# Optimization experiments

Hardware: AMD Instinct MI355X
Metric: run time of the kernel (lower is better)

## Reference

```python
import jax, jax.numpy as jnp
import numpy as np

EPS = 1e-5


def _lstm(x, W_ih, W_hh, b_ih, b_hh):
    # x: [B, T, in]; torch LSTM gate order i, f, g, o. Returns (last h, last c).
    def step(carry, xt):
        h, c = carry
        z = xt @ W_ih.T + h @ W_hh.T + (b_ih + b_hh)  # [B, 4H]
        i, f, g, o = jnp.split(z, 4, axis=-1)
        c = jax.nn.sigmoid(f) * c + jax.nn.sigmoid(i) * jnp.tanh(g)
        h = jax.nn.sigmoid(o) * jnp.tanh(c)
        return (h, c), None
    h0 = jnp.zeros((x.shape[0], W_hh.shape[1]), x.dtype)
    (h, c), _ = jax.lax.scan(step, (h0, h0), jnp.swapaxes(x, 0, 1))
    return h, c


def _bn_train(x, g, b):
    # BatchNorm1d in training mode: batch stats, biased variance.
    m = x.mean(axis=0)
    v = x.var(axis=0)
    return g * (x - m) * jax.lax.rsqrt(v + EPS) + b


def _forward(agent_traj, neighbours, aW_ih, aW_hh, ab_ih, ab_hh,
             nW_ih, nW_hh, nb_ih, nb_hh, dW_ih, dW_hh, db_ih, db_hh,
             pW, pb, rW, rb, m1W, m1b, g1, be1, m2W, m2b, g2, be2,
             i1W, i1b, ig1, ib1, i2W, i2b, ig2, ib2, segment_ids):
    B = agent_traj.shape[0]
    # relative distance: neighbour last position - owning agent's last position
    rel = neighbours[:, -1, :] - agent_traj[segment_ids, -1, :]          # [N, 2]
    agent_h, agent_c = _lstm(agent_traj, aW_ih, aW_hh, ab_ih, ab_hh)     # [B, 64]
    neigh_h, _ = _lstm(neighbours, nW_ih, nW_hh, nb_ih, nb_hh)           # [N, 64]
    rel_emb = rel @ rW.T + rb                                            # [N, 64]
    x = jnp.concatenate([neigh_h, rel_emb], axis=1)                      # [N, 128]
    x = _bn_train(jax.nn.relu(x @ m1W.T + m1b), g1, be1)                 # [N, 512]
    x = _bn_train(jax.nn.relu(x @ m2W.T + m2b), g2, be2)                 # [N, 1024]
    # per-sample max pooling over each sample's neighbours (zeros if none)
    pooled = jax.ops.segment_max(x, segment_ids, num_segments=B)         # [B, 1024]
    counts = jax.ops.segment_sum(jnp.ones((x.shape[0],), x.dtype), segment_ids, num_segments=B)
    pooled = jnp.where(counts[:, None] > 0, pooled, jnp.zeros((), x.dtype))
    d = jnp.concatenate([pooled, agent_h], axis=1)                       # [B, 1088]
    d = _bn_train(jax.nn.relu(d @ i1W.T + i1b), ig1, ib1)                # [B, 1024]
    d = _bn_train(jax.nn.relu(d @ i2W.T + i2b), ig2, ib2)                # [B, 64]

    def dec_step(carry, _):
        h, c = carry
        z = h @ dW_ih.T + h @ dW_hh.T + (db_ih + db_hh)
        i, f, g, o = jnp.split(z, 4, axis=-1)
        c = jax.nn.sigmoid(f) * c + jax.nn.sigmoid(i) * jnp.tanh(g)
        h = jax.nn.sigmoid(o) * jnp.tanh(c)
        return (h, c), h
    _, hs = jax.lax.scan(dec_step, (d, agent_c), None, length=30)        # [30, B, 64]
    pred = jnp.einsum('tbh,oh->bto', hs, pW) + pb                        # [B, 30, 2]
    return pred


def setup_inputs() -> dict:
    B, T, N, Tn, H = 2048, 20, 32768, 20, 64
    key = jax.random.key(0)
    ki = iter(jax.random.split(key, 40))
    def rn(shape, s=0.1):
        return jax.random.normal(next(ki), shape, dtype=jnp.float32) * s
    inp = dict(
        agent_traj=rn((B, T, 2), 1.0),
        neighbours=rn((N, Tn, 2), 1.0),
        aW_ih=rn((4 * H, 2)), aW_hh=rn((4 * H, H)), ab_ih=rn((4 * H,)), ab_hh=rn((4 * H,)),
        nW_ih=rn((4 * H, 2)), nW_hh=rn((4 * H, H)), nb_ih=rn((4 * H,)), nb_hh=rn((4 * H,)),
        dW_ih=rn((4 * H, H)), dW_hh=rn((4 * H, H)), db_ih=rn((4 * H,)), db_hh=rn((4 * H,)),
        pW=rn((2, H)), pb=rn((2,)),
        rW=rn((H, 2)), rb=rn((H,)),
        m1W=rn((512, 128)), m1b=rn((512,)),
        g1=jnp.ones((512,), jnp.float32), be1=jnp.zeros((512,), jnp.float32),
        m2W=rn((1024, 512)), m2b=rn((1024,)),
        g2=jnp.ones((1024,), jnp.float32), be2=jnp.zeros((1024,), jnp.float32),
        i1W=rn((1024, 1088)), i1b=rn((1024,)),
        ig1=jnp.ones((1024,), jnp.float32), ib1=jnp.zeros((1024,), jnp.float32),
        i2W=rn((H, 1024)), i2b=rn((H,)),
        ig2=jnp.ones((H,), jnp.float32), ib2=jnp.zeros((H,), jnp.float32),
        segment_ids=jnp.sort(jax.random.randint(next(ki), (N,), 0, B)).astype(jnp.int32),
    )
    return inp


def reference(agent_traj, neighbours, aW_ih, aW_hh, ab_ih, ab_hh,
              nW_ih, nW_hh, nb_ih, nb_hh, dW_ih, dW_hh, db_ih, db_hh,
              pW, pb, rW, rb, m1W, m1b, g1, be1, m2W, m2b, g2, be2,
              i1W, i1b, ig1, ib1, i2W, i2b, ig2, ib2, segment_ids):
    return _forward(agent_traj, neighbours, aW_ih, aW_hh, ab_ih, ab_hh,
                    nW_ih, nW_hh, nb_ih, nb_hh, dW_ih, dW_hh, db_ih, db_hh,
                    pW, pb, rW, rb, m1W, m1b, g1, be1, m2W, m2b, g2, be2,
                    i1W, i1b, ig1, ib1, i2W, i2b, ig2, ib2, segment_ids)
```

## Files before the change

kernel.cpp:

```cpp
#include <hip/hip_runtime.h>

#define EPS_BN 1e-5f

typedef __attribute__((ext_vector_type(8))) short short8;
typedef __attribute__((ext_vector_type(4))) float f32x4;

__device__ __forceinline__ float fast_rcp(float x) { return __builtin_amdgcn_rcpf(x); }
__device__ __forceinline__ float sigmoid_f(float x) { return fast_rcp(1.0f + __expf(-x)); }
__device__ __forceinline__ float tanh_f(float x) { return 1.0f - 2.0f * fast_rcp(__expf(2.0f * x) + 1.0f); }

__device__ __forceinline__ unsigned short f2bf(float f) {
    unsigned u = __float_as_uint(f);
    u += 0x7FFFu + ((u >> 16) & 1u);
    return (unsigned short)(u >> 16);
}
__device__ __forceinline__ unsigned pk_bf(float a, float b) {
    return (unsigned)f2bf(a) | ((unsigned)f2bf(b) << 16);
}
__device__ __forceinline__ float bf_hi(float f) {
    return __uint_as_float((unsigned)f2bf(f) << 16);
}
__device__ __forceinline__ float bf2f(unsigned short u) {
    return __uint_as_float((unsigned)u << 16);
}

__device__ __forceinline__ void gload16(const unsigned short* g, unsigned short* l) {
    __builtin_amdgcn_global_load_lds(
        (const __attribute__((address_space(1))) unsigned int*)g,
        (__attribute__((address_space(3))) unsigned int*)l,
        16, 0, 0);
}

union AFrag { short e[8]; short8 v; };
union BFrag { uint4 u; short8 v; };

__global__ __launch_bounds__(256, 2) void lstm_mfma(
    const float* __restrict__ xA,
    const float* __restrict__ aW_ih, const float* __restrict__ aW_hh,
    const float* __restrict__ ab_ih, const float* __restrict__ ab_hh,
    float* __restrict__ agent_h, float* __restrict__ agent_c,
    const float* __restrict__ xN,
    const float* __restrict__ nW_ih, const float* __restrict__ nW_hh,
    const float* __restrict__ nb_ih, const float* __restrict__ nb_hh,
    float* __restrict__ neigh_h,
    int nAgentBlk, int T)
{
    __shared__ unsigned h_ex[2][2][32 * 52];

    const bool isA = (blockIdx.x < (unsigned)nAgentBlk);
    const long blk = isA ? blockIdx.x : blockIdx.x - nAgentBlk;
    const float* __restrict__ x     = isA ? xA   : xN;
    const float* __restrict__ W_ih  = isA ? aW_ih : nW_ih;
    const float* __restrict__ W_hh  = isA ? aW_hh : nW_hh;
    const float* __restrict__ b_ih  = isA ? ab_ih : nb_ih;
    const float* __restrict__ b_hh  = isA ? ab_hh : nb_hh;
    float* __restrict__ h_out = isA ? agent_h : neigh_h;
    float* __restrict__ c_out = isA ? agent_c : nullptr;

    const int tid  = threadIdx.x;
    const int w    = tid >> 6;
    const int lane = tid & 63;
    const int s    = lane & 15;
    const int q    = lane >> 4;

    short8 ahi[4][3], alo[4][3];
#pragma unroll
    for (int gt = 0; gt < 4; ++gt) {
        const int n = gt * 64 + w * 16 + s;
#pragma unroll
        for (int kc = 0; kc < 2; ++kc) {
            const float* src = &W_hh[n * 64 + kc * 32 + q * 8];
            float4 v0 = *(const float4*)src;
            float4 v1 = *(const float4*)(src + 4);
            float v[8] = {v0.x, v0.y, v0.z, v0.w, v1.x, v1.y, v1.z, v1.w};
            AFrag a, b;
#pragma unroll
            for (int j = 0; j < 8; ++j) {
                a.e[j] = (short)f2bf(v[j]);
                b.e[j] = (short)f2bf(v[j] - bf_hi(v[j]));
            }
            ahi[gt][kc] = a.v;
            alo[gt][kc] = b.v;
        }
        AFrag a2, b2;
#pragma unroll
        for (int j = 0; j < 8; ++j) { a2.e[j] = 0; b2.e[j] = 0; }
        if (q == 0) {
            const float wi0 = W_ih[n * 2 + 0];
            const float wi1 = W_ih[n * 2 + 1];
            const float bs  = b_ih[n] + b_hh[n];
            a2.e[0] = (short)f2bf(wi0); b2.e[0] = (short)f2bf(wi0 - bf_hi(wi0));
            a2.e[1] = (short)f2bf(wi1); b2.e[1] = (short)f2bf(wi1 - bf_hi(wi1));
            a2.e[2] = (short)f2bf(bs);  b2.e[2] = (short)f2bf(bs  - bf_hi(bs));
        }
        ahi[gt][2] = a2.v;
        alo[gt][2] = b2.v;
    }

    for (int i = tid; i < 2 * 2 * 32 * 52; i += 256) (&h_ex[0][0][0])[i] = 0u;
    __syncthreads();
    if (tid < 32) {
        h_ex[0][0][tid * 52 + 33] = pk_bf(1.0f, 0.0f);
        h_ex[1][0][tid * 52 + 33] = pk_bf(1.0f, 0.0f);
        float2 xv = *(const float2*)&x[(blk * 32 + tid) * (long)(T * 2)];
        h_ex[0][0][tid * 52 + 32] = pk_bf(xv.x, xv.y);
        h_ex[0][1][tid * 52 + 32] = pk_bf(xv.x - bf_hi(xv.x), xv.y - bf_hi(xv.y));
    }
    __syncthreads();

    float creg[2][4] = {{0.f, 0.f, 0.f, 0.f}, {0.f, 0.f, 0.f, 0.f}};

    for (int t = 0; t < T; ++t) {
        const int rb = t & 1, wb = rb ^ 1;
        BFrag bhi[2][3], blo[2][3];
#pragma unroll
        for (int g = 0; g < 2; ++g)
#pragma unroll
        for (int kc = 0; kc < 3; ++kc) {
            const int off = (g * 16 + s) * 52 + kc * 16 + (q >> 1) * 8 + (q & 1) * 4;
            bhi[g][kc].u = *(const uint4*)&h_ex[rb][0][off];
            blo[g][kc].u = *(const uint4*)&h_ex[rb][1][off];
        }

        f32x4 acc[4][2];
#pragma unroll
        for (int gt = 0; gt < 4; ++gt) { acc[gt][0] = (f32x4)0.f; acc[gt][1] = (f32x4)0.f; }

#pragma unroll
        for (int kc = 0; kc < 3; ++kc) {
#pragma unroll
            for (int g = 0; g < 2; ++g) {
                const short8 bh = bhi[g][kc].v;
                const short8 bl = blo[g][kc].v;
#pragma unroll
                for (int gt = 0; gt < 4; ++gt) {
                    f32x4 a = acc[gt][g];
                    a = __builtin_amdgcn_mfma_f32_16x16x32_bf16(ahi[gt][kc], bh, a, 0, 0, 0);
                    a = __builtin_amdgcn_mfma_f32_16x16x32_bf16(ahi[gt][kc], bl, a, 0, 0, 0);
                    a = __builtin_amdgcn_mfma_f32_16x16x32_bf16(alo[gt][kc], bh, a, 0, 0, 0);
                    acc[gt][g] = a;
                }
            }
        }

#pragma unroll
        for (int g = 0; g < 2; ++g) {
            float hval[4];
#pragma unroll
            for (int r = 0; r < 4; ++r) {
                const float ei = __expf(-acc[0][g][r]);
                const float eg = __expf(2.0f * acc[2][g][r]);
                const float it = (eg - 1.0f) * fast_rcp((1.0f + ei) * (eg + 1.0f));
                const float sf = fast_rcp(1.0f + __expf(-acc[1][g][r]));
                const float c  = fmaf(sf, creg[g][r], it);
                creg[g][r] = c;
                const float eo = __expf(-acc[3][g][r]);
                const float ec = __expf(2.0f * c);
                hval[r] = (ec - 1.0f) * fast_rcp((1.0f + eo) * (ec + 1.0f));
            }
            {
                const int w0 = (g * 16 + s) * 52 + w * 8 + q * 2;
                h_ex[wb][0][w0]     = pk_bf(hval[0], hval[1]);
                h_ex[wb][0][w0 + 1] = pk_bf(hval[2], hval[3]);
                h_ex[wb][1][w0]     = pk_bf(hval[0] - bf_hi(hval[0]), hval[1] - bf_hi(hval[1]));
                h_ex[wb][1][w0 + 1] = pk_bf(hval[2] - bf_hi(hval[2]), hval[3] - bf_hi(hval[3]));
            }
            if (t == T - 1) {
                const long seq = blk * 32 + g * 16 + s;
                const int j0 = w * 16 + q * 4;
                *(float4*)&h_out[seq * 64 + j0] = make_float4(hval[0], hval[1], hval[2], hval[3]);
                if (c_out)
                    *(float4*)&c_out[seq * 64 + j0] =
                        make_float4(creg[g][0], creg[g][1], creg[g][2], creg[g][3]);
            }
        }
        if (tid < 32 && t + 1 < T) {
            float2 xv = *(const float2*)&x[(blk * 32 + tid) * (long)(T * 2) + (t + 1) * 2];
            h_ex[wb][0][tid * 52 + 32] = pk_bf(xv.x, xv.y);
            h_ex[wb][1][tid * 52 + 32] = pk_bf(xv.x - bf_hi(xv.x), xv.y - bf_hi(xv.y));
        }
        __syncthreads();
    }
}

__global__ __launch_bounds__(256) void build_x0(
    const float* __restrict__ neigh_h, const float* __restrict__ neighbours,
    const float* __restrict__ agent_traj, const int* __restrict__ seg,
    const float* __restrict__ rW, const float* __restrict__ rb,
    unsigned short* __restrict__ x0hi, unsigned short* __restrict__ x0lo, int T)
{
    const long n = (long)blockIdx.x * 2 + (threadIdx.x >> 7);
    const int j = threadIdx.x & 127;
    float v;
    if (j < 64) {
        v = neigh_h[n*64 + j];
    } else {
        const int o = j - 64;
        const int sid = seg[n];
        const float ra = neighbours[n*(long)(T*2) + (T-1)*2 + 0] - agent_traj[(long)sid*(T*2) + (T-1)*2 + 0];
        const float rbv= neighbours[n*(long)(T*2) + (T-1)*2 + 1] - agent_traj[(long)sid*(T*2) + (T-1)*2 + 1];
        v = fmaf(rW[o*2+0], ra, fmaf(rW[o*2+1], rbv, rb[o]));
    }
    x0hi[n*128 + j] = f2bf(v);
    x0lo[n*128 + j] = f2bf(v - bf_hi(v));
}

__global__ __launch_bounds__(64) void prep_wfrag(
    const float* __restrict__ W, const float* __restrict__ sc, int K,
    unsigned short* __restrict__ Whi, unsigned short* __restrict__ Wlo)
{
    const int nKc = K >> 5;
    const int blk = blockIdx.x;
    const int ti = blk / nKc, kc = blk - ti * nKc;
    const int l = threadIdx.x;
    const int n = ti * 16 + (l & 15);
    const int k0 = kc * 32 + (l >> 4) * 8;
    const long ob = ((long)blk * 64 + l) * 8;
#pragma unroll
    for (int j = 0; j < 8; ++j) {
        float v = W[(long)n * K + k0 + j];
        if (sc) v *= sc[k0 + j];
        Whi[ob + j] = f2bf(v);
        Wlo[ob + j] = f2bf(v - bf_hi(v));
    }
}

__global__ __launch_bounds__(64) void prep_bias(
    const float* __restrict__ W, const float* __restrict__ sh,
    const float* __restrict__ b, int K, float* __restrict__ bout)
{
    const int n = blockIdx.x;
    const int l = threadIdx.x;
    float s = 0.f;
    if (sh)
        for (int k = l; k < K; k += 64) s += sh[k] * W[(long)n * K + k];
#pragma unroll
    for (int m = 32; m >= 1; m >>= 1) s += __shfl_xor(s, m, 64);
    if (l == 0) bout[n] = b[n] + s;
}

__global__ __launch_bounds__(256, 2) void gemm_split(
    const unsigned short* __restrict__ Ahi,
    const unsigned short* __restrict__ Alo,
    const unsigned short* __restrict__ Whi,
    const unsigned short* __restrict__ Wlo,
    const float* __restrict__ bias,
    float* __restrict__ Yf,
    unsigned short* __restrict__ Yhi,
    unsigned short* __restrict__ Ylo,
    float* __restrict__ accum,
    const int* __restrict__ segp,
    float* __restrict__ poolmax,
    int M, int K, int O)
{
    __shared__ unsigned short As[2][2][128 * 32];
    __shared__ int segl[128];
    const int t = threadIdx.x;
    const int lane = t & 63;
    const int w = t >> 6;
    const int wm = w & 1, wn = w >> 1;

    const int nx = gridDim.x;
    const int flat = blockIdx.y * nx + blockIdx.x;
    const int grp = flat / (8 * nx);
    const int loc = flat - grp * (8 * nx);
    const int m0 = (grp * 8 + (loc & 7)) * 128;
    const int n0 = (loc >> 3) * 128;
    const int nKc = K >> 5;

    f32x4 acc[4][4];
#pragma unroll
    for (int mt = 0; mt < 4; ++mt)
#pragma unroll
    for (int nt = 0; nt < 4; ++nt) acc[mt][nt] = (f32x4)0.f;

    const int rloc0 = w * 32 + (lane >> 2);
    const int rloc1 = rloc0 + 16;
    const int sd = lane & 3;
    const unsigned short* gsrc[2][2];
    gsrc[0][0] = Ahi + (long)(m0 + rloc0) * K + (sd ^ ((rloc0 >> 1) & 3)) * 8;
    gsrc[0][1] = Ahi + (long)(m0 + rloc1) * K + (sd ^ ((rloc1 >> 1) & 3)) * 8;
    gsrc[1][0] = Alo + (long)(m0 + rloc0) * K + (sd ^ ((rloc0 >> 1) & 3)) * 8;
    gsrc[1][1] = Alo + (long)(m0 + rloc1) * K + (sd ^ ((rloc1 >> 1) & 3)) * 8;

    auto stageA = [&](int buf, int kc) {
#pragma unroll
        for (int pp = 0; pp < 2; ++pp)
#pragma unroll
        for (int cc = 0; cc < 2; ++cc)
            gload16(gsrc[pp][cc] + kc * 32,
                    &As[buf][pp][(w * 32 + cc * 16) * 32]);
    };

    const int s2 = ((lane >> 4) ^ ((lane >> 1) & 3)) * 8;
    const int arow = wm * 64 + (lane & 15);
    const long bt0 = (long)((n0 >> 4) + wn * 4);

    auto loadB = [&](BFrag* bh, BFrag* bl, int kc) {
#pragma unroll
        for (int nt = 0; nt < 4; ++nt) {
            const long fb = ((bt0 + nt) * nKc + kc) * 512 + lane * 8;
            bh[nt].u = *(const uint4*)(Whi + fb);
            bl[nt].u = *(const uint4*)(Wlo + fb);
        }
    };
    auto compute = [&](int buf, BFrag* bh, BFrag* bl) {
        BFrag afh[4], afl[4];
#pragma unroll
        for (int mt = 0; mt < 4; ++mt) {
            afh[mt].u = *(const uint4*)&As[buf][0][(arow + mt * 16) * 32 + s2];
            afl[mt].u = *(const uint4*)&As[buf][1][(arow + mt * 16) * 32 + s2];
        }
#pragma unroll
        for (int nt = 0; nt < 4; ++nt)
#pragma unroll
        for (int mt = 0; mt < 4; ++mt) {
            f32x4 a = acc[mt][nt];
            a = __builtin_amdgcn_mfma_f32_16x16x32_bf16(afh[mt].v, bh[nt].v, a, 0, 0, 0);
            a = __builtin_amdgcn_mfma_f32_16x16x32_bf16(afh[mt].v, bl[nt].v, a, 0, 0, 0);
            a = __builtin_amdgcn_mfma_f32_16x16x32_bf16(afl[mt].v, bh[nt].v, a, 0, 0, 0);
            acc[mt][nt] = a;
        }
    };

    BFrag bh0[4], bl0[4], bh1[4], bl1[4];
    stageA(0, 0);
    loadB(bh0, bl0, 0);
    __syncthreads();
    for (int kc = 0; kc < nKc; kc += 2) {
        stageA(1, kc + 1);
        loadB(bh1, bl1, kc + 1);
        compute(0, bh0, bl0);
        __syncthreads();
        if (kc + 2 < nKc) {
            stageA(0, kc + 2);
            loadB(bh0, bl0, kc + 2);
        }
        compute(1, bh1, bl1);
        if (kc + 2 < nKc) __syncthreads();
    }

    int sid0 = 0, span = 0;
    bool useLds = false;
    float* pool = nullptr;
    if (segp) {
        __syncthreads();
        if (t < 128) segl[t] = segp[m0 + t];
        __syncthreads();
        sid0 = segl[0];
        span = segl[127] - sid0 + 1;
        pool = (float*)&As[0][0][0];
        useLds = (span <= 60);
        if (useLds) {
            for (int i = t; i < span * 132; i += 256) pool[i] = 0.f;
            __syncthreads();
        }
    }

    const int cn = lane & 15, cq = lane >> 4;
#pragma unroll
    for (int nt = 0; nt < 4; ++nt) {
        const int cl = wn * 64 + nt * 16 + cn;
        const int n = n0 + cl;
        const float bs = bias[n];
        float s = 0.f, ssq = 0.f;
#pragma unroll
        for (int mt = 0; mt < 4; ++mt) {
            const int mb = wm * 64 + mt * 16 + cq * 4;
            float vmax = 0.f; int sid = -1;
#pragma unroll
            for (int r = 0; r < 4; ++r) {
                const float v = fmaxf(acc[mt][nt][r] + bs, 0.f);
                s += v; ssq += v * v;
                if (segp) {
                    const int sr = segl[mb + r];
                    if (r == 0) { vmax = v; sid = sr; }
                    else if (sr == sid) { vmax = fmaxf(vmax, v); }
                    else {
                        if (vmax > 0.f) {
                            if (useLds)
                                atomicMax((int*)&pool[(sid - sid0) * 132 + cl], __float_as_int(vmax));
                            else
                                atomicMax((int*)&poolmax[(long)sid * O + n], __float_as_int(vmax));
                        }
                        sid = sr; vmax = v;
                    }
                } else if (Yf) {
                    Yf[(long)(m0 + mb + r) * O + n] = v;
                } else {
                    const long idx = (long)(m0 + mb + r) * O + n;
                    Yhi[idx] = f2bf(v);
                    Ylo[idx] = f2bf(v - bf_hi(v));
                }
            }
            if (segp && vmax > 0.f) {
                if (useLds)
                    atomicMax((int*)&pool[(sid - sid0) * 132 + cl], __float_as_int(vmax));
                else
                    atomicMax((int*)&poolmax[(long)sid * O + n], __float_as_int(vmax));
            }
        }
        if (accum) {
            s   += __shfl_xor(s, 16, 64);   ssq += __shfl_xor(ssq, 16, 64);
            s   += __shfl_xor(s, 32, 64);   ssq += __shfl_xor(ssq, 32, 64);
            if (cq == 0) {
                atomicAdd(&accum[n], s);
                atomicAdd(&accum[O + n], ssq);
            }
        }
    }

    if (segp && useLds) {
        __syncthreads();
        for (int e = t; e < span * 128; e += 256) {
            const int sl = e >> 7, c = e & 127;
            const float v = pool[sl * 132 + c];
            const long gi = (long)(sid0 + sl) * O + (n0 + c);
            if (sl == 0 || sl == span - 1) {
                if (v > 0.f) atomicMax((int*)&poolmax[gi], __float_as_int(v));
            } else {
                poolmax[gi] = v;
            }
        }
    }
}

__global__ __launch_bounds__(256) void colstats(
    const float* __restrict__ Y, int M, int O, int chunkRows,
    float* __restrict__ accum)
{
    const int c = blockIdx.x * 64 + (threadIdx.x & 63);
    const int rgrp = threadIdx.x >> 6;
    const int r0 = blockIdx.y * chunkRows;
    int rend = r0 + chunkRows; if (rend > M) rend = M;
    float s = 0.f, ss = 0.f;
    for (int r = r0 + rgrp; r < rend; r += 4) {
        const float v = Y[(long)r*O + c];
        s += v; ss += v*v;
    }
    __shared__ float l1[256], l2[256];
    l1[threadIdx.x] = s; l2[threadIdx.x] = ss;
    __syncthreads();
    if (threadIdx.x < 64) {
        const int c2 = blockIdx.x * 64 + threadIdx.x;
        s  = l1[threadIdx.x] + l1[threadIdx.x+64] + l1[threadIdx.x+128] + l1[threadIdx.x+192];
        ss = l2[threadIdx.x] + l2[threadIdx.x+64] + l2[threadIdx.x+128] + l2[threadIdx.x+192];
        atomicAdd(&accum[c2], s);
        atomicAdd(&accum[O + c2], ss);
    }
}

__global__ __launch_bounds__(256) void bn_finalize(
    const float* __restrict__ accum, const float* __restrict__ g,
    const float* __restrict__ be, int O, float invM,
    float* __restrict__ scale, float* __restrict__ shift)
{
    const int o = blockIdx.x * 256 + threadIdx.x;
    if (o < O) {
        const float mean = accum[o] * invM;
        const float var  = accum[O + o] * invM - mean * mean;
        const float sc   = g[o] * rsqrtf(var + EPS_BN);
        scale[o] = sc;
        shift[o] = be[o] - mean * sc;
    }
}

__global__ __launch_bounds__(256) void build_d0(
    const float* __restrict__ poolraw, const float* __restrict__ agent_h,
    const int* __restrict__ seg, int N,
    const float* __restrict__ sc2, const float* __restrict__ sh2,
    unsigned short* __restrict__ d0hi, unsigned short* __restrict__ d0lo)
{
    const int b = blockIdx.x;
    int l = 0, h = N;
    while (l < h) { const int mid = (l + h) >> 1; if (seg[mid] < b) l = mid + 1; else h = mid; }
    const bool nonempty = (l < N) && (seg[l] == b);
    for (int c = threadIdx.x; c < 1088; c += 256) {
        float v;
        if (c < 1024) {
            v = nonempty ? fmaf(sc2[c], poolraw[(long)b*1024 + c], sh2[c]) : 0.f;
        } else {
            v = agent_h[(long)b*64 + (c - 1024)];
        }
        d0hi[(long)b*1088 + c] = f2bf(v);
        d0lo[(long)b*1088 + c] = f2bf(v - bf_hi(v));
    }
}

__global__ __launch_bounds__(256) void gemm_i2_part(
    const float* __restrict__ A,
    const float* __restrict__ W,
    const float* __restrict__ ascale, const float* __restrict__ ashift,
    float* __restrict__ part, int M, int K, int kchunk)
{
    __shared__ float As[16][132];
    __shared__ float Bs[16][68];
    const int t = threadIdx.x;
    const int m0 = blockIdx.x * 128;
    const int ks = blockIdx.y;
    const int kbeg = ks * kchunk;
    const int kend = kbeg + kchunk;
    const int tm = (t & 15) * 8;
    const int tn = (t >> 4) * 4;
    const int ar = t >> 1;
    const int ac = (t & 1) * 8;
    const int br = t >> 2;
    const int bc = (t & 3) * 4;

    float acc[8][4];
#pragma unroll
    for (int i = 0; i < 8; ++i)
#pragma unroll
    for (int j = 0; j < 4; ++j) acc[i][j] = 0.f;

    for (int k0 = kbeg; k0 < kend; k0 += 16) {
        float4 a0 = *(const float4*)&A[(long)(m0+ar)*K + k0 + ac];
        float4 a1 = *(const float4*)&A[(long)(m0+ar)*K + k0 + ac + 4];
        float4 s0 = *(const float4*)&ascale[k0 + ac];
        float4 s1 = *(const float4*)&ascale[k0 + ac + 4];
        float4 h0 = *(const float4*)&ashift[k0 + ac];
        float4 h1 = *(const float4*)&ashift[k0 + ac + 4];
        a0.x = fmaf(a0.x, s0.x, h0.x); a0.y = fmaf(a0.y, s0.y, h0.y);
        a0.z = fmaf(a0.z, s0.z, h0.z); a0.w = fmaf(a0.w, s0.w, h0.w);
        a1.x = fmaf(a1.x, s1.x, h1.x); a1.y = fmaf(a1.y, s1.y, h1.y);
        a1.z = fmaf(a1.z, s1.z, h1.z); a1.w = fmaf(a1.w, s1.w, h1.w);
        float4 b0 = *(const float4*)&W[(long)br*K + k0 + bc];
        __syncthreads();
        As[ac+0][ar] = a0.x; As[ac+1][ar] = a0.y; As[ac+2][ar] = a0.z; As[ac+3][ar] = a0.w;
        As[ac+4][ar] = a1.x; As[ac+5][ar] = a1.y; As[ac+6][ar] = a1.z; As[ac+7][ar] = a1.w;
        Bs[bc+0][br] = b0.x; Bs[bc+1][br] = b0.y; Bs[bc+2][br] = b0.z; Bs[bc+3][br] = b0.w;
        __syncthreads();
#pragma unroll
        for (int kk = 0; kk < 16; ++kk) {
            float av[8], bv[4];
            *(float4*)&av[0] = *(const float4*)&As[kk][tm];
            *(float4*)&av[4] = *(const float4*)&As[kk][tm + 4];
            *(float4*)&bv[0] = *(const float4*)&Bs[kk][tn];
#pragma unroll
            for (int i = 0; i < 8; ++i)
#pragma unroll
            for (int j = 0; j < 4; ++j)
                acc[i][j] = fmaf(av[i], bv[j], acc[i][j]);
        }
    }

    float* po = part + (long)ks * M * 64;
#pragma unroll
    for (int i = 0; i < 8; ++i)
        *(float4*)&po[(long)(m0 + tm + i) * 64 + tn] = *(float4*)&acc[i][0];
}

__global__ __launch_bounds__(256) void i2_finish(
    const float* __restrict__ part, const float* __restrict__ bias,
    int M, int KS, float* __restrict__ t2)
{
    const long idx = (long)blockIdx.x * 256 + threadIdx.x;
    if (idx < (long)M * 64) {
        float s = 0.f;
        for (int ks = 0; ks < KS; ++ks) s += part[(long)ks * M * 64 + idx];
        t2[idx] = fmaxf(s + bias[idx & 63], 0.f);
    }
}

__global__ __launch_bounds__(256) void prep_dec(
    const float* __restrict__ dW_ih, const float* __restrict__ dW_hh,
    const float* __restrict__ db_ih, const float* __restrict__ db_hh,
    float* __restrict__ Wc, float* __restrict__ bc)
{
    const int idx = blockIdx.x * 256 + threadIdx.x;
    if (idx < 256*64) Wc[idx] = dW_ih[idx] + dW_hh[idx];
    else if (idx < 256*64 + 256) bc[idx - 256*64] = db_ih[idx - 256*64] + db_hh[idx - 256*64];
}

__global__ __launch_bounds__(256) void decoder_kernel(
    const float* __restrict__ t2, const float* __restrict__ sc4,
    const float* __restrict__ sh4, const float* __restrict__ agent_c,
    const float* __restrict__ Wc, const float* __restrict__ bc,
    const float* __restrict__ pW, const float* __restrict__ pb,
    float* __restrict__ pred )
{
    __shared__ float h_lds[2][64];
    __shared__ float zg_lds[2][64];
    __shared__ float zo_lds[2][64];
    const int t = threadIdx.x;
    const int lane = t & 63;
    const int wave = t >> 6;
    const int s = wave >> 1;
    const int role = wave & 1;
    const long seq = (long)blockIdx.x * 2 + s;

    const int r0 = role * 128 + lane;
    const int r1 = r0 + 64;
    float w0[64], w1[64];
#pragma unroll
    for (int k = 0; k < 64; k += 4) {
        float4 va = *(const float4*)&Wc[r0 * 64 + k];
        w0[k] = va.x; w0[k+1] = va.y; w0[k+2] = va.z; w0[k+3] = va.w;
        float4 vb = *(const float4*)&Wc[r1 * 64 + k];
        w1[k] = vb.x; w1[k+1] = vb.y; w1[k+2] = vb.z; w1[k+3] = vb.w;
    }
    const float bias0 = bc[r0];
    const float bias1 = bc[r1];
    const float pw0 = pW[lane], pw1 = pW[64 + lane];
    const float pb0 = pb[0], pb1 = pb[1];

    float c = agent_c[seq*64 + lane];
    if (role == 0)
        h_lds[s][lane] = fmaf(sc4[lane], t2[seq*64 + lane], sh4[lane]);
    __syncthreads();
    float hv = h_lds[s][lane];

    for (int step = 0; step < 30; ++step) {
        float z0 = bias0, z1 = bias1;
#pragma unroll
        for (int k = 0; k < 64; ++k) {
            float hk = __int_as_float(__builtin_amdgcn_readlane(__float_as_int(hv), k));
            z0 = fmaf(hk, w0[k], z0);
            z1 = fmaf(hk, w1[k], z1);
        }
        if (role == 1) { zg_lds[s][lane] = z0; zo_lds[s][lane] = z1; }
        __syncthreads();
        if (role == 0) {
            const float ig = sigmoid_f(z0);
            const float fg = sigmoid_f(z1);
            const float gg = tanh_f(zg_lds[s][lane]);
            const float og = sigmoid_f(zo_lds[s][lane]);
            c = fmaf(fg, c, ig * gg);
            h_lds[s][lane] = og * tanh_f(c);
        }
        __syncthreads();
        hv = h_lds[s][lane];
        if (role == 0) {
            float p0 = hv * pw0;
            float p1 = hv * pw1;
#pragma unroll
            for (int m = 32; m >= 1; m >>= 1) {
                p0 += __shfl_xor(p0, m, 64);
                p1 += __shfl_xor(p1, m, 64);
            }
            if (lane == 0) {
                pred[seq*60 + step*2 + 0] = p0 + pb0;
                pred[seq*60 + step*2 + 1] = p1 + pb1;
            }
        }
    }
}

extern "C" void kernel_launch(void* const* d_in, const int* in_sizes, int n_in,
                              void* d_out, int out_size, void* d_ws, size_t ws_size,
                              hipStream_t stream)
{
    const float* agent_traj = (const float*)d_in[0];
    const float* neighbours = (const float*)d_in[1];
    const float* aW_ih = (const float*)d_in[2];
    const float* aW_hh = (const float*)d_in[3];
    const float* ab_ih = (const float*)d_in[4];
    const float* ab_hh = (const float*)d_in[5];
    const float* nW_ih = (const float*)d_in[6];
    const float* nW_hh = (const float*)d_in[7];
    const float* nb_ih = (const float*)d_in[8];
    const float* nb_hh = (const float*)d_in[9];
    const float* dW_ih = (const float*)d_in[10];
    const float* dW_hh = (const float*)d_in[11];
    const float* db_ih = (const float*)d_in[12];
    const float* db_hh = (const float*)d_in[13];
    const float* pW = (const float*)d_in[14];
    const float* pb = (const float*)d_in[15];
    const float* rW = (const float*)d_in[16];
    const float* rb = (const float*)d_in[17];
    const float* m1W = (const float*)d_in[18];
    const float* m1b = (const float*)d_in[19];
    const float* g1  = (const float*)d_in[20];
    const float* be1 = (const float*)d_in[21];
    const float* m2W = (const float*)d_in[22];
    const float* m2b = (const float*)d_in[23];
    const float* g2  = (const float*)d_in[24];
    const float* be2 = (const float*)d_in[25];
    const float* i1W = (const float*)d_in[26];
    const float* i1b = (const float*)d_in[27];
    const float* ig1 = (const float*)d_in[28];
    const float* ib1 = (const float*)d_in[29];
    const float* i2W = (const float*)d_in[30];
    const float* i2b = (const float*)d_in[31];
    const float* ig2 = (const float*)d_in[32];
    const float* ib2 = (const float*)d_in[33];
    const int*   seg = (const int*)d_in[34];
    float* pred = (float*)d_out;

    const int B = 2048, T = 20, N = 32768;

    char* p = (char*)d_ws;
    auto alloc = [&](size_t bytes) -> char* {
        char* r = p; p += (bytes + 255) & ~(size_t)255; return r;
    };
    float* agent_h = (float*)alloc((size_t)B*64*4);
    float* agent_c = (float*)alloc((size_t)B*64*4);
    char* neigh_region = alloc((size_t)N*64*4);
    unsigned short* x0hi = (unsigned short*)alloc((size_t)N*128*2);
    unsigned short* x0lo = (unsigned short*)alloc((size_t)N*128*2);
    char* y1hi_region  = alloc((size_t)N*512*2);
    unsigned short* y1lo = (unsigned short*)alloc((size_t)N*512*2);
    float* poolraw = (float*)alloc((size_t)B*1024*4);
    float* accAll = (float*)alloc((size_t)(1024+2048+2048+128)*4);
    float* acc1 = accAll;
    float* acc2 = accAll + 1024;
    float* acc3 = accAll + 3072;
    float* acc4 = accAll + 5120;
    float* sc1 = (float*)alloc(512*4);  float* sh1 = (float*)alloc(512*4);
    float* sc2 = (float*)alloc(1024*4); float* sh2 = (float*)alloc(1024*4);
    float* sc3 = (float*)alloc(1024*4); float* sh3 = (float*)alloc(1024*4);
    float* sc4 = (float*)alloc(64*4);   float* sh4 = (float*)alloc(64*4);
    float* Wc = (float*)alloc(256*64*4);
    float* bc = (float*)alloc(256*4);
    unsigned short* W1hi = (unsigned short*)alloc((size_t)512*128*2);
    unsigned short* W1lo = (unsigned short*)alloc((size_t)512*128*2);
    unsigned short* W2hi = (unsigned short*)alloc((size_t)1024*512*2);
    unsigned short* W2lo = (unsigned short*)alloc((size_t)1024*512*2);
    unsigned short* Wi1hi = (unsigned short*)alloc((size_t)1024*1088*2);
    unsigned short* Wi1lo = (unsigned short*)alloc((size_t)1024*1088*2);
    float* b1f = (float*)alloc(512*4);
    float* b2f = (float*)alloc(1024*4);
    float* bi1f = (float*)alloc(1024*4);
    float* i2part = (float*)alloc((size_t)8*B*64*4);

    float* neigh_h = (float*)neigh_region;
    float* t1      = (float*)neigh_region;
    unsigned short* y1hi = (unsigned short*)y1hi_region;
    unsigned short* d0hi = (unsigned short*)y1hi_region;
    unsigned short* d0lo = d0hi + (size_t)B*1088;
    float* t2 = (float*)(y1hi_region + (size_t)2*B*1088*2);

    hipMemsetAsync(accAll, 0, (1024+2048+2048+128)*sizeof(float), stream);
    hipMemsetAsync(poolraw, 0, (size_t)B*1024*4, stream);

    prep_wfrag<<<(512/16)*(128/32), 64, 0, stream>>>(m1W, nullptr, 128, W1hi, W1lo);
    prep_bias<<<512, 64, 0, stream>>>(m1W, nullptr, m1b, 128, b1f);
    prep_wfrag<<<(1024/16)*(1088/32), 64, 0, stream>>>(i1W, nullptr, 1088, Wi1hi, Wi1lo);
    prep_bias<<<1024, 64, 0, stream>>>(i1W, nullptr, i1b, 1088, bi1f);
    prep_dec<<<65, 256, 0, stream>>>(dW_ih, dW_hh, db_ih, db_hh, Wc, bc);

    lstm_mfma<<<B/32 + N/32, 256, 0, stream>>>(
        agent_traj, aW_ih, aW_hh, ab_ih, ab_hh, agent_h, agent_c,
        neighbours, nW_ih, nW_hh, nb_ih, nb_hh, neigh_h,
        B/32, T);
    build_x0<<<N/2, 256, 0, stream>>>(neigh_h, neighbours, agent_traj, seg, rW, rb,
                                      x0hi, x0lo, T);

    gemm_split<<<dim3(512/128, N/128), 256, 0, stream>>>(
        x0hi, x0lo, W1hi, W1lo, b1f, nullptr, y1hi, y1lo, acc1,
        nullptr, nullptr, N, 128, 512);
    bn_finalize<<<2, 256, 0, stream>>>(acc1, g1, be1, 512, 1.0f/N, sc1, sh1);

    prep_wfrag<<<(1024/16)*(512/32), 64, 0, stream>>>(m2W, sc1, 512, W2hi, W2lo);
    prep_bias<<<1024, 64, 0, stream>>>(m2W, sh1, m2b, 512, b2f);

    gemm_split<<<dim3(1024/128, N/128), 256, 0, stream>>>(
        y1hi, y1lo, W2hi, W2lo, b2f, nullptr, nullptr, nullptr, acc2,
        seg, poolraw, N, 512, 1024);
    bn_finalize<<<4, 256, 0, stream>>>(acc2, g2, be2, 1024, 1.0f/N, sc2, sh2);

    build_d0<<<B, 256, 0, stream>>>(poolraw, agent_h, seg, N, sc2, sh2, d0hi, d0lo);

    gemm_split<<<dim3(1024/128, B/128), 256, 0, stream>>>(
        d0hi, d0lo, Wi1hi, Wi1lo, bi1f, t1, nullptr, nullptr, acc3,
        nullptr, nullptr, B, 1088, 1024);
    bn_finalize<<<4, 256, 0, stream>>>(acc3, ig1, ib1, 1024, 1.0f/B, sc3, sh3);

    gemm_i2_part<<<dim3(B/128, 8), 256, 0, stream>>>(t1, i2W, sc3, sh3, i2part,
                                                     B, 1024, 128);
    i2_finish<<<(B*64)/256, 256, 0, stream>>>(i2part, i2b, B, 8, t2);
    colstats<<<dim3(1, 8), 256, 0, stream>>>(t2, B, 64, 256, acc4);
    bn_finalize<<<1, 256, 0, stream>>>(acc4, ig2, ib2, 64, 1.0f/B, sc4, sh4);

    decoder_kernel<<<B/2, 256, 0, stream>>>(t2, sc4, sh4, agent_c, Wc, bc, pW, pb, pred);
}
```

Measured before the change: 610.8 us.

## Fuse prep, build_x0, and BN-finalize kernels into neighbouring launches

Merges the weight/bias prep launches into one prep_all kernel and writes the neighbour LSTM's final hidden state plus the relative-position embedding directly as bf16 hi/lo x0 inside the LSTM kernel. It removes the separate build_x0, bn_finalize (for layers 1, 2 and 4), colstats and prep_dec launches. Batch-norm scale and shift are now recomputed inline from the accumulated sums in their consumer kernels, and the last layer's column stats are accumulated inside i2_finish. The goal is fewer kernel launches and less intermediate traffic, at the cost of some redundant per-element rsqrt work. i2_finish_stats assumes B*64 is a multiple of 2048.

```diff
diff --git a/kernel.cpp b/kernel.cpp
--- a/kernel.cpp
+++ b/kernel.cpp
@@ -19,9 +19,6 @@
 }
 __device__ __forceinline__ float bf_hi(float f) {
     return __uint_as_float((unsigned)f2bf(f) << 16);
-}
-__device__ __forceinline__ float bf2f(unsigned short u) {
-    return __uint_as_float((unsigned)u << 16);
 }
 
 __device__ __forceinline__ void gload16(const unsigned short* g, unsigned short* l) {
@@ -42,7 +39,9 @@
     const float* __restrict__ xN,
     const float* __restrict__ nW_ih, const float* __restrict__ nW_hh,
     const float* __restrict__ nb_ih, const float* __restrict__ nb_hh,
-    float* __restrict__ neigh_h,
+    const int* __restrict__ seg, const float* __restrict__ rW,
+    const float* __restrict__ rb,
+    unsigned short* __restrict__ x0hi, unsigned short* __restrict__ x0lo,
     int nAgentBlk, int T)
 {
     __shared__ unsigned h_ex[2][2][32 * 52];
@@ -54,8 +53,6 @@
     const float* __restrict__ W_hh  = isA ? aW_hh : nW_hh;
     const float* __restrict__ b_ih  = isA ? ab_ih : nb_ih;
     const float* __restrict__ b_hh  = isA ? ab_hh : nb_hh;
-    float* __restrict__ h_out = isA ? agent_h : neigh_h;
-    float* __restrict__ c_out = isA ? agent_c : nullptr;
 
     const int tid  = threadIdx.x;
     const int w    = tid >> 6;
@@ -111,15 +108,15 @@
     float creg[2][4] = {{0.f, 0.f, 0.f, 0.f}, {0.f, 0.f, 0.f, 0.f}};
 
     for (int t = 0; t < T; ++t) {
-        const int rb = t & 1, wb = rb ^ 1;
+        const int rb_ = t & 1, wb = rb_ ^ 1;
         BFrag bhi[2][3], blo[2][3];
 #pragma unroll
         for (int g = 0; g < 2; ++g)
 #pragma unroll
         for (int kc = 0; kc < 3; ++kc) {
             const int off = (g * 16 + s) * 52 + kc * 16 + (q >> 1) * 8 + (q & 1) * 4;
-            bhi[g][kc].u = *(const uint4*)&h_ex[rb][0][off];
-            blo[g][kc].u = *(const uint4*)&h_ex[rb][1][off];
+            bhi[g][kc].u = *(const uint4*)&h_ex[rb_][0][off];
+            blo[g][kc].u = *(const uint4*)&h_ex[rb_][1][off];
         }
 
         f32x4 acc[4][2];
@@ -168,10 +165,18 @@
             if (t == T - 1) {
                 const long seq = blk * 32 + g * 16 + s;
                 const int j0 = w * 16 + q * 4;
-                *(float4*)&h_out[seq * 64 + j0] = make_float4(hval[0], hval[1], hval[2], hval[3]);
-                if (c_out)
-                    *(float4*)&c_out[seq * 64 + j0] =
+                if (isA) {
+                    *(float4*)&agent_h[seq * 64 + j0] =
+                        make_float4(hval[0], hval[1], hval[2], hval[3]);
+                    *(float4*)&agent_c[seq * 64 + j0] =
                         make_float4(creg[g][0], creg[g][1], creg[g][2], creg[g][3]);
+                } else {
+                    *(uint2*)&x0hi[seq * 128 + j0] = make_uint2(
+                        pk_bf(hval[0], hval[1]), pk_bf(hval[2], hval[3]));
+                    *(uint2*)&x0lo[seq * 128 + j0] = make_uint2(
+                        pk_bf(hval[0] - bf_hi(hval[0]), hval[1] - bf_hi(hval[1])),
+                        pk_bf(hval[2] - bf_hi(hval[2]), hval[3] - bf_hi(hval[3])));
+                }
             }
         }
         if (tid < 32 && t + 1 < T) {
@@ -181,62 +186,111 @@
         }
         __syncthreads();
     }
-}
-
-__global__ __launch_bounds__(256) void build_x0(
-    const float* __restrict__ neigh_h, const float* __restrict__ neighbours,
-    const float* __restrict__ agent_traj, const int* __restrict__ seg,
-    const float* __restrict__ rW, const float* __restrict__ rb,
-    unsigned short* __restrict__ x0hi, unsigned short* __restrict__ x0lo, int T)
-{
-    const long n = (long)blockIdx.x * 2 + (threadIdx.x >> 7);
-    const int j = threadIdx.x & 127;
-    float v;
-    if (j < 64) {
-        v = neigh_h[n*64 + j];
-    } else {
-        const int o = j - 64;
+
+    if (!isA) {
+        const int sloc = tid >> 3;
+        const long n = blk * 32 + sloc;
+        const float2 np = *(const float2*)&x[n * (long)(T * 2) + (T - 1) * 2];
         const int sid = seg[n];
-        const float ra = neighbours[n*(long)(T*2) + (T-1)*2 + 0] - agent_traj[(long)sid*(T*2) + (T-1)*2 + 0];
-        const float rbv= neighbours[n*(long)(T*2) + (T-1)*2 + 1] - agent_traj[(long)sid*(T*2) + (T-1)*2 + 1];
-        v = fmaf(rW[o*2+0], ra, fmaf(rW[o*2+1], rbv, rb[o]));
-    }
-    x0hi[n*128 + j] = f2bf(v);
-    x0lo[n*128 + j] = f2bf(v - bf_hi(v));
-}
-
-__global__ __launch_bounds__(64) void prep_wfrag(
-    const float* __restrict__ W, const float* __restrict__ sc, int K,
+        const float2 ap = *(const float2*)&xA[(long)sid * (T * 2) + (T - 1) * 2];
+        const float ra = np.x - ap.x, rbv = np.y - ap.y;
+        const int o0 = (tid & 7) * 8;
+#pragma unroll
+        for (int j = 0; j < 8; ++j) {
+            const int o = o0 + j;
+            const float v = fmaf(rW[o * 2 + 0], ra, fmaf(rW[o * 2 + 1], rbv, rb[o]));
+            x0hi[n * 128 + 64 + o] = f2bf(v);
+            x0lo[n * 128 + 64 + o] = f2bf(v - bf_hi(v));
+        }
+    }
+}
+
+__device__ __forceinline__ void wfrag_body(
+    const float* __restrict__ W, int K, int blk, int l,
     unsigned short* __restrict__ Whi, unsigned short* __restrict__ Wlo)
 {
     const int nKc = K >> 5;
-    const int blk = blockIdx.x;
     const int ti = blk / nKc, kc = blk - ti * nKc;
-    const int l = threadIdx.x;
     const int n = ti * 16 + (l & 15);
     const int k0 = kc * 32 + (l >> 4) * 8;
     const long ob = ((long)blk * 64 + l) * 8;
 #pragma unroll
     for (int j = 0; j < 8; ++j) {
         float v = W[(long)n * K + k0 + j];
-        if (sc) v *= sc[k0 + j];
         Whi[ob + j] = f2bf(v);
         Wlo[ob + j] = f2bf(v - bf_hi(v));
     }
 }
 
-__global__ __launch_bounds__(64) void prep_bias(
-    const float* __restrict__ W, const float* __restrict__ sh,
-    const float* __restrict__ b, int K, float* __restrict__ bout)
-{
-    const int n = blockIdx.x;
-    const int l = threadIdx.x;
-    float s = 0.f;
-    if (sh)
-        for (int k = l; k < K; k += 64) s += sh[k] * W[(long)n * K + k];
-#pragma unroll
-    for (int m = 32; m >= 1; m >>= 1) s += __shfl_xor(s, m, 64);
-    if (l == 0) bout[n] = b[n] + s;
+__global__ __launch_bounds__(64) void prep_all(
+    const float* __restrict__ m1W, const float* __restrict__ m1b,
+    const float* __restrict__ i1W, const float* __restrict__ i1b,
+    const float* __restrict__ dW_ih, const float* __restrict__ dW_hh,
+    const float* __restrict__ db_ih, const float* __restrict__ db_hh,
+    unsigned short* __restrict__ W1hi, unsigned short* __restrict__ W1lo,
+    float* __restrict__ b1f,
+    unsigned short* __restrict__ Wi1hi, unsigned short* __restrict__ Wi1lo,
+    float* __restrict__ bi1f,
+    float* __restrict__ Wc, float* __restrict__ bc)
+{
+    const int b = blockIdx.x, l = threadIdx.x;
+    if (b < 128) {
+        wfrag_body(m1W, 128, b, l, W1hi, W1lo);
+    } else if (b < 2304) {
+        wfrag_body(i1W, 1088, b - 128, l, Wi1hi, Wi1lo);
+    } else if (b < 2312) {
+        const int i = (b - 2304) * 64 + l;
+        b1f[i] = m1b[i];
+    } else if (b < 2328) {
+        const int i = (b - 2312) * 64 + l;
+        bi1f[i] = i1b[i];
+    } else {
+        const int idx = (b - 2328) * 64 + l;
+        if (idx < 16384) Wc[idx] = dW_ih[idx] + dW_hh[idx];
+        else if (idx < 16640) bc[idx - 16384] = db_ih[idx - 16384] + db_hh[idx - 16384];
+    }
+}
+
+__global__ __launch_bounds__(64) void prep_w2(
+    const float* __restrict__ W,
+    const float* __restrict__ b2,
+    const float* __restrict__ acc1,
+    const float* __restrict__ g1, const float* __restrict__ be1,
+    float invN,
+    unsigned short* __restrict__ Whi, unsigned short* __restrict__ Wlo,
+    float* __restrict__ bout)
+{
+    const int K = 512, nKc = 16;
+    const int blk = blockIdx.x, l = threadIdx.x;
+    if (blk < 1024) {
+        const int ti = blk / nKc, kc = blk - ti * nKc;
+        const int n = ti * 16 + (l & 15);
+        const int k0 = kc * 32 + (l >> 4) * 8;
+        const long ob = ((long)blk * 64 + l) * 8;
+#pragma unroll
+        for (int j = 0; j < 8; ++j) {
+            const int k = k0 + j;
+            const float mean = acc1[k] * invN;
+            const float var  = acc1[512 + k] * invN - mean * mean;
+            const float sc   = g1[k] * rsqrtf(var + EPS_BN);
+            const float v = W[(long)n * K + k] * sc;
+            Whi[ob + j] = f2bf(v);
+            Wlo[ob + j] = f2bf(v - bf_hi(v));
+        }
+    } else {
+        const int n = blk - 1024;
+        float s = 0.f;
+        for (int k = l; k < K; k += 64) {
+            const float mean = acc1[k] * invN;
+            const float var  = acc1[512 + k] * invN - mean * mean;
+            const float sc   = g1[k] * rsqrtf(var + EPS_BN);
+            const float sh   = be1[k] - mean * sc;
+            s += sh * W[(long)n * K + k];
+        }
+#pragma unroll
+        for (int m = 32; m >= 1; m >>= 1) s += __shfl_xor(s, m, 64);
+        if (l == 0) bout[n] = b2[n] + s;
+    }
 }
 
 __global__ __launch_bounds__(256, 2) void gemm_split(
@@ -425,31 +479,6 @@
     }
 }
 
-__global__ __launch_bounds__(256) void colstats(
-    const float* __restrict__ Y, int M, int O, int chunkRows,
-    float* __restrict__ accum)
-{
-    const int c = blockIdx.x * 64 + (threadIdx.x & 63);
-    const int rgrp = threadIdx.x >> 6;
-    const int r0 = blockIdx.y * chunkRows;
-    int rend = r0 + chunkRows; if (rend > M) rend = M;
-    float s = 0.f, ss = 0.f;
-    for (int r = r0 + rgrp; r < rend; r += 4) {
-        const float v = Y[(long)r*O + c];
-        s += v; ss += v*v;
-    }
-    __shared__ float l1[256], l2[256];
-    l1[threadIdx.x] = s; l2[threadIdx.x] = ss;
-    __syncthreads();
-    if (threadIdx.x < 64) {
-        const int c2 = blockIdx.x * 64 + threadIdx.x;
-        s  = l1[threadIdx.x] + l1[threadIdx.x+64] + l1[threadIdx.x+128] + l1[threadIdx.x+192];
-        ss = l2[threadIdx.x] + l2[threadIdx.x+64] + l2[threadIdx.x+128] + l2[threadIdx.x+192];
-        atomicAdd(&accum[c2], s);
-        atomicAdd(&accum[O + c2], ss);
-    }
-}
-
 __global__ __launch_bounds__(256) void bn_finalize(
     const float* __restrict__ accum, const float* __restrict__ g,
     const float* __restrict__ be, int O, float invM,
@@ -468,7 +497,8 @@
 __global__ __launch_bounds__(256) void build_d0(
     const float* __restrict__ poolraw, const float* __restrict__ agent_h,
     const int* __restrict__ seg, int N,
-    const float* __restrict__ sc2, const float* __restrict__ sh2,
+    const float* __restrict__ acc2, const float* __restrict__ g2,
+    const float* __restrict__ be2, float invN,
     unsigned short* __restrict__ d0hi, unsigned short* __restrict__ d0lo)
 {
     const int b = blockIdx.x;
@@ -478,12 +508,16 @@
     for (int c = threadIdx.x; c < 1088; c += 256) {
         float v;
         if (c < 1024) {
-            v = nonempty ? fmaf(sc2[c], poolraw[(long)b*1024 + c], sh2[c]) : 0.f;
+            const float mean = acc2[c] * invN;
+            const float var  = acc2[1024 + c] * invN - mean * mean;
+            const float sc   = g2[c] * rsqrtf(var + EPS_BN);
+            const float sh   = be2[c] - mean * sc;
+            v = nonempty ? fmaf(sc, poolraw[(long)b * 1024 + c], sh) : 0.f;
         } else {
-            v = agent_h[(long)b*64 + (c - 1024)];
-        }
-        d0hi[(long)b*1088 + c] = f2bf(v);
-        d0lo[(long)b*1088 + c] = f2bf(v - bf_hi(v));
+            v = agent_h[(long)b * 64 + (c - 1024)];
+        }
+        d0hi[(long)b * 1088 + c] = f2bf(v);
+        d0lo[(long)b * 1088 + c] = f2bf(v - bf_hi(v));
     }
 }
 
@@ -550,31 +584,37 @@
         *(float4*)&po[(long)(m0 + tm + i) * 64 + tn] = *(float4*)&acc[i][0];
 }
 
-__global__ __launch_bounds__(256) void i2_finish(
+__global__ __launch_bounds__(256) void i2_finish_stats(
     const float* __restrict__ part, const float* __restrict__ bias,
-    int M, int KS, float* __restrict__ t2)
-{
-    const long idx = (long)blockIdx.x * 256 + threadIdx.x;
-    if (idx < (long)M * 64) {
-        float s = 0.f;
-        for (int ks = 0; ks < KS; ++ks) s += part[(long)ks * M * 64 + idx];
-        t2[idx] = fmaxf(s + bias[idx & 63], 0.f);
-    }
-}
-
-__global__ __launch_bounds__(256) void prep_dec(
-    const float* __restrict__ dW_ih, const float* __restrict__ dW_hh,
-    const float* __restrict__ db_ih, const float* __restrict__ db_hh,
-    float* __restrict__ Wc, float* __restrict__ bc)
-{
-    const int idx = blockIdx.x * 256 + threadIdx.x;
-    if (idx < 256*64) Wc[idx] = dW_ih[idx] + dW_hh[idx];
-    else if (idx < 256*64 + 256) bc[idx - 256*64] = db_ih[idx - 256*64] + db_hh[idx - 256*64];
+    int M, int KS, float* __restrict__ t2, float* __restrict__ accum)
+{
+    __shared__ float l1[256], l2[256];
+    const int t = threadIdx.x;
+    const long base = (long)blockIdx.x * 2048;
+    float s = 0.f, ss = 0.f;
+#pragma unroll
+    for (int k = 0; k < 8; ++k) {
+        const long idx = base + k * 256 + t;
+        float v = 0.f;
+        for (int ks = 0; ks < KS; ++ks) v += part[(long)ks * M * 64 + idx];
+        v = fmaxf(v + bias[idx & 63], 0.f);
+        t2[idx] = v;
+        s += v; ss += v * v;
+    }
+    l1[t] = s; l2[t] = ss;
+    __syncthreads();
+    if (t < 64) {
+        s  = l1[t] + l1[t + 64] + l1[t + 128] + l1[t + 192];
+        ss = l2[t] + l2[t + 64] + l2[t + 128] + l2[t + 192];
+        atomicAdd(&accum[t], s);
+        atomicAdd(&accum[64 + t], ss);
+    }
 }
 
 __global__ __launch_bounds__(256) void decoder_kernel(
-    const float* __restrict__ t2, const float* __restrict__ sc4,
-    const float* __restrict__ sh4, const float* __restrict__ agent_c,
+    const float* __restrict__ t2, const float* __restrict__ acc4,
+    const float* __restrict__ ig2, const float* __restrict__ ib2, float invB,
+    const float* __restrict__ agent_c,
     const float* __restrict__ Wc, const float* __restrict__ bc,
     const float* __restrict__ pW, const float* __restrict__ pb,
     float* __restrict__ pred )
@@ -605,8 +645,13 @@
     const float pb0 = pb[0], pb1 = pb[1];
 
     float c = agent_c[seq*64 + lane];
-    if (role == 0)
-        h_lds[s][lane] = fmaf(sc4[lane], t2[seq*64 + lane], sh4[lane]);
+    if (role == 0) {
+        const float mean = acc4[lane] * invB;
+        const float var  = acc4[64 + lane] * invB - mean * mean;
+        const float sc   = ig2[lane] * rsqrtf(var + EPS_BN);
+        const float sh   = ib2[lane] - mean * sc;
+        h_lds[s][lane] = fmaf(sc, t2[seq*64 + lane], sh);
+    }
     __syncthreads();
     float hv = h_lds[s][lane];
 
@@ -706,10 +751,7 @@
     float* acc2 = accAll + 1024;
     float* acc3 = accAll + 3072;
     float* acc4 = accAll + 5120;
-    float* sc1 = (float*)alloc(512*4);  float* sh1 = (float*)alloc(512*4);
-    float* sc2 = (float*)alloc(1024*4); float* sh2 = (float*)alloc(1024*4);
     float* sc3 = (float*)alloc(1024*4); float* sh3 = (float*)alloc(1024*4);
-    float* sc4 = (float*)alloc(64*4);   float* sh4 = (float*)alloc(64*4);
     float* Wc = (float*)alloc(256*64*4);
     float* bc = (float*)alloc(256*4);
     unsigned short* W1hi = (unsigned short*)alloc((size_t)512*128*2);
@@ -723,8 +765,7 @@
     float* bi1f = (float*)alloc(1024*4);
     float* i2part = (float*)alloc((size_t)8*B*64*4);
 
-    float* neigh_h = (float*)neigh_region;
-    float* t1      = (float*)neigh_region;
+    float* t1 = (float*)neigh_region;
     unsigned short* y1hi = (unsigned short*)y1hi_region;
     unsigned short* d0hi = (unsigned short*)y1hi_region;
     unsigned short* d0lo = d0hi + (size_t)B*1088;
@@ -733,33 +774,27 @@
     hipMemsetAsync(accAll, 0, (1024+2048+2048+128)*sizeof(float), stream);
     hipMemsetAsync(poolraw, 0, (size_t)B*1024*4, stream);
 
-    prep_wfrag<<<(512/16)*(128/32), 64, 0, stream>>>(m1W, nullptr, 128, W1hi, W1lo);
-    prep_bias<<<512, 64, 0, stream>>>(m1W, nullptr, m1b, 128, b1f);
-    prep_wfrag<<<(1024/16)*(1088/32), 64, 0, stream>>>(i1W, nullptr, 1088, Wi1hi, Wi1lo);
-    prep_bias<<<1024, 64, 0, stream>>>(i1W, nullptr, i1b, 1088, bi1f);
-    prep_dec<<<65, 256, 0, stream>>>(dW_ih, dW_hh, db_ih, db_hh, Wc, bc);
+    prep_all<<<2588, 64, 0, stream>>>(m1W, m1b, i1W, i1b, dW_ih, dW_hh, db_ih, db_hh,
+                                      W1hi, W1lo, b1f, Wi1hi, Wi1lo, bi1f, Wc, bc);
 
     lstm_mfma<<<B/32 + N/32, 256, 0, stream>>>(
         agent_traj, aW_ih, aW_hh, ab_ih, ab_hh, agent_h, agent_c,
-        neighbours, nW_ih, nW_hh, nb_ih, nb_hh, neigh_h,
-        B/32, T);
-    build_x0<<<N/2, 256, 0, stream>>>(neigh_h, neighbours, agent_traj, seg, rW, rb,
-                                      x0hi, x0lo, T);
+        neighbours, nW_ih, nW_hh, nb_ih, nb_hh,
+        seg, rW, rb, x0hi, x0lo, B/32, T);
 
     gemm_split<<<dim3(512/128, N/128), 256, 0, stream>>>(
         x0hi, x0lo, W1hi, W1lo, b1f, nullptr, y1hi, y1lo, acc1,
         nullptr, nullptr, N, 128, 512);
-    bn_finalize<<<2, 256, 0, stream>>>(acc1, g1, be1, 512, 1.0f/N, sc1, sh1);
-
-    prep_wfrag<<<(1024/16)*(512/32), 64, 0, stream>>>(m2W, sc1, 512, W2hi, W2lo);
-    prep_bias<<<1024, 64, 0, stream>>>(m2W, sh1, m2b, 512, b2f);
+
+    prep_w2<<<2048, 64, 0, stream>>>(m2W, m2b, acc1, g1, be1, 1.0f/N,
+                                     W2hi, W2lo, b2f);
 
     gemm_split<<<dim3(1024/128, N/128), 256, 0, stream>>>(
         y1hi, y1lo, W2hi, W2lo, b2f, nullptr, nullptr, nullptr, acc2,
         seg, poolraw, N, 512, 1024);
-    bn_finalize<<<4, 256, 0, stream>>>(acc2, g2, be2, 1024, 1.0f/N, sc2, sh2);
-
-    build_d0<<<B, 256, 0, stream>>>(poolraw, agent_h, seg, N, sc2, sh2, d0hi, d0lo);
+
+    build_d0<<<B, 256, 0, stream>>>(poolraw, agent_h, seg, N, acc2, g2, be2,
+                                    1.0f/N, d0hi, d0lo);
 
     gemm_split<<<dim3(1024/128, B/128), 256, 0, stream>>>(
         d0hi, d0lo, Wi1hi, Wi1lo, bi1f, t1, nullptr, nullptr, acc3,
@@ -768,9 +803,8 @@
 
     gemm_i2_part<<<dim3(B/128, 8), 256, 0, stream>>>(t1, i2W, sc3, sh3, i2part,
                                                      B, 1024, 128);
-    i2_finish<<<(B*64)/256, 256, 0, stream>>>(i2part, i2b, B, 8, t2);
-    colstats<<<dim3(1, 8), 256, 0, stream>>>(t2, B, 64, 256, acc4);
-    bn_finalize<<<1, 256, 0, stream>>>(acc4, ig2, ib2, 64, 1.0f/B, sc4, sh4);
-
-    decoder_kernel<<<B/2, 256, 0, stream>>>(t2, sc4, sh4, agent_c, Wc, bc, pW, pb, pred);
-}
+    i2_finish_stats<<<64, 256, 0, stream>>>(i2part, i2b, B, 8, t2, acc4);
+
+    decoder_kernel<<<B/2, 256, 0, stream>>>(t2, acc4, ig2, ib2, 1.0f/B,
+                                            agent_c, Wc, bc, pW, pb, pred);
+}
```

Measured after the change: 581.4 us, median of 2. 1.05x faster.
